# Optimization experiments

Measured on AMD Instinct MI355X. Metric: run time of the kernel, lower is better.

The kernel has to match this reference:

```python
import jax, jax.numpy as jnp
import numpy as np

HID = 128

def _gru_states(x, w_ih, w_hh, b_ih, b_hh):
    # x: [B,T,I]; w_ih: [3H,I]; w_hh: [3H,H]; biases: [3H]
    # Precompute input projections for all timesteps (one big GEMM).
    gi = jnp.einsum('bti,gi->tbg', x, w_ih) + b_ih  # [T,B,3H]
    B = x.shape[0]
    h0 = jnp.zeros((B, HID), dtype=x.dtype)

    def step(h, gi_t):
        gh = h @ w_hh.T + b_hh                      # [B,3H]
        i_r, i_z, i_n = jnp.split(gi_t, 3, axis=-1)
        h_r, h_z, h_n = jnp.split(gh, 3, axis=-1)
        r = jax.nn.sigmoid(i_r + h_r)
        z = jax.nn.sigmoid(i_z + h_z)
        n = jnp.tanh(i_n + r * h_n)
        h_new = (1.0 - z) * n + z * h
        return h_new, h_new

    _, states = jax.lax.scan(step, h0, gi)          # states: [T,B,H]
    return states


def setup_inputs() -> dict:
    key = jax.random.key(0)
    ks = jax.random.split(key, 7)
    B, T, I, H, E = 64, 2048, 128, HID, 64
    s_ih = 1.0 / np.sqrt(I)
    s_hh = 1.0 / np.sqrt(H)
    s_p = 1.0 / np.sqrt(H)
    return {
        'x': jax.random.normal(ks[0], (B, T, I), dtype=jnp.float32),
        'w_ih': jax.random.uniform(ks[1], (3 * H, I), jnp.float32, -s_ih, s_ih),
        'w_hh': jax.random.uniform(ks[2], (3 * H, H), jnp.float32, -s_hh, s_hh),
        'b_ih': jax.random.uniform(ks[3], (3 * H,), jnp.float32, -s_hh, s_hh),
        'b_hh': jax.random.uniform(ks[4], (3 * H,), jnp.float32, -s_hh, s_hh),
        'w_proj': jax.random.uniform(ks[5], (E, H), jnp.float32, -s_p, s_p),
        'b_proj': jax.random.uniform(ks[6], (E,), jnp.float32, -s_p, s_p),
    }


def reference(x, w_ih, w_hh, b_ih, b_hh, w_proj, b_proj):
    states = _gru_states(x, w_ih, w_hh, b_ih, b_hh)  # [T,B,H]
    pooled = states.mean(axis=0)                     # mean pooling over time -> [B,H]
    return pooled @ w_proj.T + b_proj                # [B,E]
```

## Files before the change

kernel.cpp:

```cpp
#include <hip/hip_runtime.h>
#include <math.h>

#define B_   64
#define T_   2048
#define HID_ 128
#define G3_  384
#define IN_  128
#define E_   64

#define TS_  128
#define CT_  256

typedef _Float16 f16x8 __attribute__((ext_vector_type(8)));
typedef float    f32x4 __attribute__((ext_vector_type(4)));

#define L2E  1.4426950408889634f
#define L2E2 2.8853900817779268f

#if __has_builtin(__builtin_amdgcn_exp2f)
#define EXP2(x) __builtin_amdgcn_exp2f(x)
#else
#define EXP2(x) __expf((x) * 0.6931471805599453f)
#endif

__device__ __forceinline__ float rcp_(float x) { return __builtin_amdgcn_rcpf(x); }

__device__ __forceinline__ f16x8 pack8_(float4 a, float4 b) {
    uint4 u;
    u.x = __builtin_bit_cast(unsigned, __builtin_amdgcn_cvt_pkrtz(a.x, a.y));
    u.y = __builtin_bit_cast(unsigned, __builtin_amdgcn_cvt_pkrtz(a.z, a.w));
    u.z = __builtin_bit_cast(unsigned, __builtin_amdgcn_cvt_pkrtz(b.x, b.y));
    u.w = __builtin_bit_cast(unsigned, __builtin_amdgcn_cvt_pkrtz(b.z, b.w));
    return __builtin_bit_cast(f16x8, u);
}

__device__ __forceinline__ void gemm_body(
    int g, int nTiles, int t0,
    const float* __restrict__ x, const float* __restrict__ w_ih,
    const float* __restrict__ b_ih, const float* __restrict__ b_hh,
    float* __restrict__ gi)
{
    const int tid = threadIdx.x;
    const int w   = tid >> 6;
    const int l   = tid & 63;
    const int ln  = l & 15;
    const int kq  = l >> 4;
    const int tt  = g % nTiles;
    const int b   = g / nTiles;
    const int tl_base = tt * TS_ + w * 16;

    const float* xb = x + ((size_t)b * T_ + (size_t)(t0 + tl_base)) * IN_;

    f16x8 afr[4];
    #pragma unroll
    for (int kc = 0; kc < 4; kc++) {
        const float* xr = xb + (size_t)ln * IN_ + kc * 32 + kq * 8;
        float4 p0 = *reinterpret_cast<const float4*>(xr);
        float4 p1 = *reinterpret_cast<const float4*>(xr + 4);
        afr[kc] = pack8_(p0, p1);
    }

    #pragma unroll
    for (int half = 0; half < 2; half++) {
        f32x4 acc[12];
        #pragma unroll
        for (int j = 0; j < 12; j++) acc[j] = (f32x4){0.f, 0.f, 0.f, 0.f};

        #pragma unroll
        for (int kc = 0; kc < 4; kc++) {
            #pragma unroll
            for (int j = 0; j < 12; j++) {
                const int nt = half * 12 + j;
                const float* wr = w_ih + (size_t)(nt * 16 + ln) * IN_ + kc * 32 + kq * 8;
                float4 q0 = *reinterpret_cast<const float4*>(wr);
                float4 q1 = *reinterpret_cast<const float4*>(wr + 4);
                const f16x8 bfr = pack8_(q0, q1);
                acc[j] = __builtin_amdgcn_mfma_f32_16x16x32_f16(afr[kc], bfr, acc[j], 0, 0, 0);
            }
        }

        #pragma unroll
        for (int j = 0; j < 12; j++) {
            const int col = half * 192 + j * 16 + ln;
            const float bias = b_ih[col] + (col < 256 ? b_hh[col] : 0.f);
            #pragma unroll
            for (int r = 0; r < 4; r++) {
                const size_t trow = (size_t)(tl_base + kq * 4 + r);
                gi[trow * (B_ * G3_) + (size_t)b * G3_ + col] = acc[j][r] + bias;
            }
        }
    }
}

#define REC_STEP(CUR, LD, TLOAD, PB)                                           \
  {                                                                            \
    const char* hb_ = (const char*)(&h2_sh[PB][0]) + kq * 16;                  \
    f16x8 af_[4];                                                              \
    af_[0] = __builtin_bit_cast(f16x8, *(const uint4*)(hb_));                  \
    af_[1] = __builtin_bit_cast(f16x8, *(const uint4*)(hb_ + 64));             \
    af_[2] = __builtin_bit_cast(f16x8, *(const uint4*)(hb_ + 128));            \
    af_[3] = __builtin_bit_cast(f16x8, *(const uint4*)(hb_ + 192));            \
    const float* gp_ = gib + (size_t)(TLOAD) * S;                              \
    LD[0] = gp_[cg]; LD[1] = gp_[cg + 128]; LD[2] = gp_[cg + 256];             \
    f32x4 ac_[3];                                                              \
    _Pragma("unroll")                                                          \
    for (int g = 0; g < 3; g++) ac_[g] = (f32x4){0.f, 0.f, 0.f, 0.f};          \
    _Pragma("unroll")                                                          \
    for (int kc = 0; kc < 4; kc++) {                                           \
      _Pragma("unroll")                                                        \
      for (int g = 0; g < 3; g++)                                              \
        ac_[g] = __builtin_amdgcn_mfma_f32_16x16x32_f16(af_[kc], wf[g][kc],    \
                                                        ac_[g], 0, 0, 0);      \
    }                                                                          \
    const float q_  = CUR[2] * L2E2;                                           \
    const float yr_ = fmaf(CUR[0], L2E, ac_[0][0]);                            \
    const float r_  = rcp_(1.f + EXP2(-yr_));                                  \
    const float yz_ = fmaf(CUR[1], L2E, ac_[1][0]);                            \
    const float z_  = rcp_(1.f + EXP2(-yz_));                                  \
    const float yn_ = fmaf(r_, ac_[2][0] + bh, q_);                            \
    const float u_  = rcp_(1.f + EXP2(yn_));                                   \
    const float n_  = fmaf(-2.f, u_, 1.f);                                     \
    hj = n_ + z_ * (hj - n_);                                                  \
    hs += hj;                                                                  \
    if (kq == 0) h2_sh[(PB) ^ 1][cg] = (_Float16)hj;                           \
    __syncthreads();                                                           \
  }

__device__ __forceinline__ void rec_body(
    int b,
    const float* __restrict__ gi, const float* __restrict__ w_hh,
    const float* __restrict__ b_hh,
    const float* __restrict__ w_proj, const float* __restrict__ b_proj,
    float* __restrict__ out, float* __restrict__ state,
    int t0, int t1)
{
    const int tid  = threadIdx.x;
    const int w    = tid >> 6;
    const int lane = tid & 63;
    const int ln   = lane & 15;
    const int kq   = lane >> 4;
    const int wh   = w & 3;
    const int f    = w >> 2;
    const int cg   = 16 * wh + ln + 64 * f;
    const int nT   = t1 - t0;

    __shared__ _Float16 h2_sh[2][HID_];
    __shared__ float pooled[HID_];

    f16x8 wf[3][4];
    #pragma unroll
    for (int g = 0; g < 3; g++) {
        const float s = (g == 2) ? L2E2 : L2E;
        const float* wr = w_hh + (size_t)(128 * g + cg) * HID_;
        #pragma unroll
        for (int kc = 0; kc < 4; kc++) {
            const float* p = wr + kc * 32 + kq * 8;
            float4 q0 = *reinterpret_cast<const float4*>(p);
            float4 q1 = *reinterpret_cast<const float4*>(p + 4);
            q0.x *= s; q0.y *= s; q0.z *= s; q0.w *= s;
            q1.x *= s; q1.y *= s; q1.z *= s; q1.w *= s;
            wf[g][kc] = pack8_(q0, q1);
        }
    }
    const float bh = L2E2 * b_hh[256 + cg];

    float hj, hs;
    if (t0 == 0) { hj = hs = 0.f; }
    else {
        hj = state[b * HID_ + cg];
        hs = state[B_ * HID_ + b * HID_ + cg];
    }
    if (kq == 0) h2_sh[0][cg] = (_Float16)hj;
    __syncthreads();

    const float* gib = gi + (size_t)b * G3_;
    const size_t S = (size_t)B_ * G3_;

    float g0[3], g1[3], g2[3], g3[3];
    {
        const float* p0 = gib;
        const float* p1 = gib + S;
        g0[0] = p0[cg]; g0[1] = p0[cg + 128]; g0[2] = p0[cg + 256];
        g1[0] = p1[cg]; g1[1] = p1[cg + 128]; g1[2] = p1[cg + 256];
    }

    int pb = 0;
    const int nTm1 = nT - 1;
    for (int t = 0; t < nT; t += 4) {
        int t2 = t + 2 < nTm1 ? t + 2 : nTm1;
        int t3 = t + 3 < nTm1 ? t + 3 : nTm1;
        int t4 = t + 4 < nTm1 ? t + 4 : nTm1;
        int t5 = t + 5 < nTm1 ? t + 5 : nTm1;
        REC_STEP(g0, g2, t2, pb); pb ^= 1;
        REC_STEP(g1, g3, t3, pb); pb ^= 1;
        REC_STEP(g2, g0, t4, pb); pb ^= 1;
        REC_STEP(g3, g1, t5, pb); pb ^= 1;
    }

    if (t1 < T_) {
        if (kq == 0) {
            state[b * HID_ + cg]             = hj;
            state[B_ * HID_ + b * HID_ + cg] = hs;
        }
    } else {
        if (kq == 0) pooled[cg] = hs * (1.f / (float)T_);
        __syncthreads();
        if (tid < E_) {
            const float4* wpj = reinterpret_cast<const float4*>(w_proj + (size_t)tid * HID_);
            const float4* pp  = reinterpret_cast<const float4*>(pooled);
            float a0 = 0.f, a1 = 0.f, a2 = 0.f, a3 = 0.f;
            #pragma unroll
            for (int k = 0; k < 32; k++) {
                float4 wv = wpj[k]; float4 pv = pp[k];
                a0 = fmaf(wv.x, pv.x, a0);
                a1 = fmaf(wv.y, pv.y, a1);
                a2 = fmaf(wv.z, pv.z, a2);
                a3 = fmaf(wv.w, pv.w, a3);
            }
            out[b * E_ + tid] = (a0 + a1) + (a2 + a3) + b_proj[tid];
        }
    }
}

__global__ __launch_bounds__(512, 1)
void fused(const float* __restrict__ x, const float* __restrict__ w_ih,
           const float* __restrict__ b_ih, const float* __restrict__ w_hh,
           const float* __restrict__ b_hh,
           const float* __restrict__ w_proj, const float* __restrict__ b_proj,
           const float* __restrict__ gi_rec, float* __restrict__ gi_out,
           float* __restrict__ out, float* __restrict__ state,
           int trec0, int trec1, int tg0, int nRec, int nTiles)
{
    const int bid = (int)blockIdx.x;
    if (bid < nRec) {
        rec_body(bid, gi_rec, w_hh, b_hh, w_proj, b_proj, out, state, trec0, trec1);
    } else {
        gemm_body(bid - nRec, nTiles, tg0, x, w_ih, b_ih, b_hh, gi_out);
    }
}

extern "C" void kernel_launch(void* const* d_in, const int* in_sizes, int n_in,
                              void* d_out, int out_size, void* d_ws, size_t ws_size,
                              hipStream_t stream)
{
    const float* x      = (const float*)d_in[0];
    const float* w_ih   = (const float*)d_in[1];
    const float* w_hh   = (const float*)d_in[2];
    const float* b_ih   = (const float*)d_in[3];
    const float* b_hh   = (const float*)d_in[4];
    const float* w_proj = (const float*)d_in[5];
    const float* b_proj = (const float*)d_in[6];
    float* out = (float*)d_out;

    const size_t state_bytes = (size_t)2 * B_ * HID_ * sizeof(float);
    const size_t per_t = (size_t)B_ * G3_ * sizeof(float);

    if (ws_size >= 2 * (size_t)CT_ * per_t + state_bytes) {
        float* buf[2] = { (float*)d_ws,
                          (float*)((char*)d_ws + (size_t)CT_ * per_t) };
        float* state  = (float*)((char*)d_ws + 2 * (size_t)CT_ * per_t);
        const int nTiles = CT_ / TS_;
        const int nC = T_ / CT_;
        for (int i = 0; i <= nC; i++) {
            const int rb = (i > 0)  ? B_ : 0;
            const int gb = (i < nC) ? nTiles * B_ : 0;
            fused<<<dim3(rb + gb), dim3(512), 0, stream>>>(
                x, w_ih, b_ih, w_hh, b_hh, w_proj, b_proj,
                buf[(i + 1) & 1] , buf[i & 1],
                out, state,
                (i - 1) * CT_, i * CT_, i * CT_, rb, nTiles);
        }
    } else {
        size_t avail = ws_size > state_bytes ? ws_size - state_bytes : 0;
        int cT = (int)(avail / per_t);
        if (cT > T_) cT = T_;
        cT &= ~(TS_ - 1);
        if (cT < TS_) cT = TS_;
        float* buf0  = (float*)d_ws;
        float* state = (float*)((char*)d_ws + (size_t)cT * per_t);
        for (int t0 = 0; t0 < T_; t0 += cT) {
            int t1 = t0 + cT; if (t1 > T_) t1 = T_;
            int nt = t1 - t0;
            fused<<<dim3((nt / TS_) * B_), dim3(512), 0, stream>>>(
                x, w_ih, b_ih, w_hh, b_hh, w_proj, b_proj,
                buf0, buf0, out, state, 0, 0, t0, 0, nt / TS_);
            fused<<<dim3(B_), dim3(512), 0, stream>>>(
                x, w_ih, b_ih, w_hh, b_hh, w_proj, b_proj,
                buf0, buf0, out, state, t0, t1, 0, B_, nt / TS_);
        }
    }
}
```

Before: 861.1 us.

## Replace chunked multi-launch pipeline with single persistent launch using atomic chunk counters

Instead of launching one fused kernel per 256-step chunk, the code now issues a single launch. 64 recurrence blocks and 192 persistent producer blocks share it, and producers write the full input-projection buffer, signalling per-chunk completion with release atomics. Recurrence blocks spin on acquire loads until the current and next chunks are ready, which removes the per-launch overhead and the barrier between launches. A large dynamic LDS allocation forces one block per CU so the recurrence blocks get dedicated CUs, and the MFMA chain is split into two accumulators to shorten the dependency. It relies on all blocks being co-resident and needs a larger workspace for the full buffer.

```diff
diff --git a/kernel.cpp b/kernel.cpp
--- a/kernel.cpp
+++ b/kernel.cpp
@@ -8,8 +8,10 @@
 #define IN_  128
 #define E_   64
 
-#define TS_  128
-#define CT_  256
+#define TS_      128
+#define NCHUNK_  (T_ / TS_)
+#define NPROD_   192
+#define POLL_TGT 512
 
 typedef _Float16 f16x8 __attribute__((ext_vector_type(8)));
 typedef float    f32x4 __attribute__((ext_vector_type(4)));
@@ -35,18 +37,16 @@
 }
 
 __device__ __forceinline__ void gemm_body(
-    int g, int nTiles, int t0,
+    int tt, int b, int t0,
     const float* __restrict__ x, const float* __restrict__ w_ih,
     const float* __restrict__ b_ih, const float* __restrict__ b_hh,
-    float* __restrict__ gi)
+    float* gi)
 {
     const int tid = threadIdx.x;
     const int w   = tid >> 6;
     const int l   = tid & 63;
     const int ln  = l & 15;
     const int kq  = l >> 4;
-    const int tt  = g % nTiles;
-    const int b   = g / nTiles;
     const int tl_base = tt * TS_ + w * 16;
 
     const float* xb = x + ((size_t)b * T_ + (size_t)(t0 + tl_base)) * IN_;
@@ -102,22 +102,30 @@
     af_[3] = __builtin_bit_cast(f16x8, *(const uint4*)(hb_ + 192));            \
     const float* gp_ = gib + (size_t)(TLOAD) * S;                              \
     LD[0] = gp_[cg]; LD[1] = gp_[cg + 128]; LD[2] = gp_[cg + 256];             \
-    f32x4 ac_[3];                                                              \
-    _Pragma("unroll")                                                          \
-    for (int g = 0; g < 3; g++) ac_[g] = (f32x4){0.f, 0.f, 0.f, 0.f};          \
-    _Pragma("unroll")                                                          \
-    for (int kc = 0; kc < 4; kc++) {                                           \
-      _Pragma("unroll")                                                        \
-      for (int g = 0; g < 3; g++)                                              \
-        ac_[g] = __builtin_amdgcn_mfma_f32_16x16x32_f16(af_[kc], wf[g][kc],    \
-                                                        ac_[g], 0, 0, 0);      \
+    f32x4 aA_[3], aB_[3];                                                      \
+    _Pragma("unroll")                                                          \
+    for (int g = 0; g < 3; g++) {                                              \
+      aA_[g] = (f32x4){0.f, 0.f, 0.f, 0.f};                                    \
+      aB_[g] = (f32x4){0.f, 0.f, 0.f, 0.f};                                    \
     }                                                                          \
+    _Pragma("unroll")                                                          \
+    for (int g = 0; g < 3; g++)                                                \
+      aA_[g] = __builtin_amdgcn_mfma_f32_16x16x32_f16(af_[0], wf[g][0], aA_[g], 0, 0, 0); \
+    _Pragma("unroll")                                                          \
+    for (int g = 0; g < 3; g++)                                                \
+      aB_[g] = __builtin_amdgcn_mfma_f32_16x16x32_f16(af_[1], wf[g][1], aB_[g], 0, 0, 0); \
+    _Pragma("unroll")                                                          \
+    for (int g = 0; g < 3; g++)                                                \
+      aA_[g] = __builtin_amdgcn_mfma_f32_16x16x32_f16(af_[2], wf[g][2], aA_[g], 0, 0, 0); \
+    _Pragma("unroll")                                                          \
+    for (int g = 0; g < 3; g++)                                                \
+      aB_[g] = __builtin_amdgcn_mfma_f32_16x16x32_f16(af_[3], wf[g][3], aB_[g], 0, 0, 0); \
     const float q_  = CUR[2] * L2E2;                                           \
-    const float yr_ = fmaf(CUR[0], L2E, ac_[0][0]);                            \
+    const float yr_ = fmaf(CUR[0], L2E, aA_[0][0] + aB_[0][0]);                \
     const float r_  = rcp_(1.f + EXP2(-yr_));                                  \
-    const float yz_ = fmaf(CUR[1], L2E, ac_[1][0]);                            \
+    const float yz_ = fmaf(CUR[1], L2E, aA_[1][0] + aB_[1][0]);                \
     const float z_  = rcp_(1.f + EXP2(-yz_));                                  \
-    const float yn_ = fmaf(r_, ac_[2][0] + bh, q_);                            \
+    const float yn_ = fmaf(r_, aA_[2][0] + aB_[2][0] + bh, q_);                \
     const float u_  = rcp_(1.f + EXP2(yn_));                                   \
     const float n_  = fmaf(-2.f, u_, 1.f);                                     \
     hj = n_ + z_ * (hj - n_);                                                  \
@@ -128,11 +136,11 @@
 
 __device__ __forceinline__ void rec_body(
     int b,
-    const float* __restrict__ gi, const float* __restrict__ w_hh,
+    const float* gi, const float* __restrict__ w_hh,
     const float* __restrict__ b_hh,
     const float* __restrict__ w_proj, const float* __restrict__ b_proj,
     float* __restrict__ out, float* __restrict__ state,
-    int t0, int t1)
+    int t0, int t1, const int* ctr)
 {
     const int tid  = threadIdx.x;
     const int w    = tid >> 6;
@@ -177,24 +185,38 @@
     const size_t S = (size_t)B_ * G3_;
 
     float g0[3], g1[3], g2[3], g3[3];
-    {
-        const float* p0 = gib;
-        const float* p1 = gib + S;
-        g0[0] = p0[cg]; g0[1] = p0[cg + 128]; g0[2] = p0[cg + 256];
-        g1[0] = p1[cg]; g1[1] = p1[cg + 128]; g1[2] = p1[cg + 256];
-    }
-
     int pb = 0;
     const int nTm1 = nT - 1;
-    for (int t = 0; t < nT; t += 4) {
-        int t2 = t + 2 < nTm1 ? t + 2 : nTm1;
-        int t3 = t + 3 < nTm1 ? t + 3 : nTm1;
-        int t4 = t + 4 < nTm1 ? t + 4 : nTm1;
-        int t5 = t + 5 < nTm1 ? t + 5 : nTm1;
-        REC_STEP(g0, g2, t2, pb); pb ^= 1;
-        REC_STEP(g1, g3, t3, pb); pb ^= 1;
-        REC_STEP(g2, g0, t4, pb); pb ^= 1;
-        REC_STEP(g3, g1, t5, pb); pb ^= 1;
+    const int nC = nT >> 7;
+
+    for (int c = 0; c < nC; c++) {
+        if (ctr) {
+            const int cw = (c + 1 < NCHUNK_) ? c + 1 : NCHUNK_ - 1;
+            while (__hip_atomic_load(&ctr[c], __ATOMIC_ACQUIRE,
+                                     __HIP_MEMORY_SCOPE_AGENT) < POLL_TGT)
+                __builtin_amdgcn_s_sleep(8);
+            while (__hip_atomic_load(&ctr[cw], __ATOMIC_ACQUIRE,
+                                     __HIP_MEMORY_SCOPE_AGENT) < POLL_TGT)
+                __builtin_amdgcn_s_sleep(8);
+        }
+        if (c == 0) {
+            const float* p0 = gib;
+            const float* p1 = gib + S;
+            g0[0] = p0[cg]; g0[1] = p0[cg + 128]; g0[2] = p0[cg + 256];
+            g1[0] = p1[cg]; g1[1] = p1[cg + 128]; g1[2] = p1[cg + 256];
+        }
+        const int tb = c << 7;
+        for (int tg = 0; tg < TS_; tg += 4) {
+            const int t = tb + tg;
+            int t2 = t + 2 < nTm1 ? t + 2 : nTm1;
+            int t3 = t + 3 < nTm1 ? t + 3 : nTm1;
+            int t4 = t + 4 < nTm1 ? t + 4 : nTm1;
+            int t5 = t + 5 < nTm1 ? t + 5 : nTm1;
+            REC_STEP(g0, g2, t2, pb); pb ^= 1;
+            REC_STEP(g1, g3, t3, pb); pb ^= 1;
+            REC_STEP(g2, g0, t4, pb); pb ^= 1;
+            REC_STEP(g3, g1, t5, pb); pb ^= 1;
+        }
     }
 
     if (t1 < T_) {
@@ -227,15 +249,24 @@
            const float* __restrict__ b_ih, const float* __restrict__ w_hh,
            const float* __restrict__ b_hh,
            const float* __restrict__ w_proj, const float* __restrict__ b_proj,
-           const float* __restrict__ gi_rec, float* __restrict__ gi_out,
-           float* __restrict__ out, float* __restrict__ state,
-           int trec0, int trec1, int tg0, int nRec, int nTiles)
+           const float* gi_rec, float* gi_out,
+           float* out, float* state, int* ctr,
+           int trec0, int trec1, int nRec, int nProd, int nJobs, int tg0)
 {
+    extern __shared__ char lds_pad_[];
+    (void)lds_pad_;
     const int bid = (int)blockIdx.x;
     if (bid < nRec) {
-        rec_body(bid, gi_rec, w_hh, b_hh, w_proj, b_proj, out, state, trec0, trec1);
+        rec_body(bid, gi_rec, w_hh, b_hh, w_proj, b_proj, out, state,
+                 trec0, trec1, ctr);
     } else {
-        gemm_body(bid - nRec, nTiles, tg0, x, w_ih, b_ih, b_hh, gi_out);
+        const int p = bid - nRec;
+        for (int j = p; j < nJobs; j += nProd) {
+            gemm_body(j >> 6, j & 63, tg0, x, w_ih, b_ih, b_hh, gi_out);
+            if (ctr && (threadIdx.x & 63) == 0)
+                __hip_atomic_fetch_add(&ctr[j >> 6], 1, __ATOMIC_RELEASE,
+                                       __HIP_MEMORY_SCOPE_AGENT);
+        }
     }
 }
 
@@ -254,22 +285,17 @@
 
     const size_t state_bytes = (size_t)2 * B_ * HID_ * sizeof(float);
     const size_t per_t = (size_t)B_ * G3_ * sizeof(float);
-
-    if (ws_size >= 2 * (size_t)CT_ * per_t + state_bytes) {
-        float* buf[2] = { (float*)d_ws,
-                          (float*)((char*)d_ws + (size_t)CT_ * per_t) };
-        float* state  = (float*)((char*)d_ws + 2 * (size_t)CT_ * per_t);
-        const int nTiles = CT_ / TS_;
-        const int nC = T_ / CT_;
-        for (int i = 0; i <= nC; i++) {
-            const int rb = (i > 0)  ? B_ : 0;
-            const int gb = (i < nC) ? nTiles * B_ : 0;
-            fused<<<dim3(rb + gb), dim3(512), 0, stream>>>(
-                x, w_ih, b_ih, w_hh, b_hh, w_proj, b_proj,
-                buf[(i + 1) & 1] , buf[i & 1],
-                out, state,
-                (i - 1) * CT_, i * CT_, i * CT_, rb, nTiles);
-        }
+    const size_t gi_bytes = (size_t)T_ * per_t;
+
+    if (ws_size >= gi_bytes + 256 + state_bytes) {
+        float* gi    = (float*)d_ws;
+        int*   ctr   = (int*)((char*)d_ws + gi_bytes);
+        float* state = (float*)((char*)d_ws + gi_bytes + 256);
+        hipMemsetAsync(ctr, 0, NCHUNK_ * sizeof(int), stream);
+        fused<<<dim3(B_ + NPROD_), dim3(512), 80 * 1024, stream>>>(
+            x, w_ih, b_ih, w_hh, b_hh, w_proj, b_proj,
+            gi, gi, out, state, ctr,
+            0, T_, B_, NPROD_, NCHUNK_ * B_, 0);
     } else {
         size_t avail = ws_size > state_bytes ? ws_size - state_bytes : 0;
         int cT = (int)(avail / per_t);
@@ -280,13 +306,15 @@
         float* state = (float*)((char*)d_ws + (size_t)cT * per_t);
         for (int t0 = 0; t0 < T_; t0 += cT) {
             int t1 = t0 + cT; if (t1 > T_) t1 = T_;
-            int nt = t1 - t0;
-            fused<<<dim3((nt / TS_) * B_), dim3(512), 0, stream>>>(
+            const int jobs = ((t1 - t0) / TS_) * B_;
+            fused<<<dim3(jobs), dim3(512), 0, stream>>>(
                 x, w_ih, b_ih, w_hh, b_hh, w_proj, b_proj,
-                buf0, buf0, out, state, 0, 0, t0, 0, nt / TS_);
+                buf0, buf0, out, state, nullptr,
+                0, 0, 0, jobs, jobs, t0);
             fused<<<dim3(B_), dim3(512), 0, stream>>>(
                 x, w_ih, b_ih, w_hh, b_hh, w_proj, b_proj,
-                buf0, buf0, out, state, t0, t1, 0, B_, nt / TS_);
-        }
-    }
-}
+                buf0, buf0, out, state, nullptr,
+                t0, t1, B_, 1, 0, 0);
+        }
+    }
+}
```

After: 1.264 ms. 1.47x slower.
